# Kernel tuning notes

Measured on AMD Instinct MI355X. Metric: run time of the kernel, lower is better.

## Reference

```python
import jax, jax.numpy as jnp
import numpy as np

N, E, B = 50000, 800000, 64
IN, H, OUT = 64, 128, 64


def _gcn_norm(edge_index, num_nodes):
    # PyG gcn_norm with add_self_loops=True: A_hat = A + I, norm = d^-1/2[src]*d^-1/2[dst]
    loop = jnp.arange(num_nodes)
    src = jnp.concatenate([edge_index[0], loop])
    dst = jnp.concatenate([edge_index[1], loop])
    deg = jax.ops.segment_sum(jnp.ones_like(dst, dtype=jnp.float32), dst,
                              num_segments=num_nodes)  # >= 1 due to self-loops
    dis = deg ** -0.5
    norm = dis[src] * dis[dst]  # [E+N]
    return src, dst, norm


def _gcn_layer(x, W, b, src, dst, norm, num_nodes):
    h = x @ W                                   # linear first (GCNConv order)
    msg = h[src] * norm[:, None]                # gather + normalize, [E+N, H]
    out = jax.ops.segment_sum(msg, dst, num_segments=num_nodes)  # scatter-add
    return out + b


def setup_inputs() -> dict:
    key = jax.random.key(0)
    ks = jax.random.split(key, 12)
    x = jax.random.normal(ks[0], (N, IN), dtype=jnp.float32)
    edge_index = jax.random.randint(ks[1], (2, E), 0, N, dtype=jnp.int64)
    batch = jnp.sort(jax.random.randint(ks[2], (N,), 0, B, dtype=jnp.int64))

    def lin(k, fan_in, fan_out):
        s = 1.0 / np.sqrt(fan_in)
        return jax.random.uniform(k, (fan_in, fan_out), jnp.float32, -s, s)

    return {
        "x": x, "edge_index": edge_index, "batch": batch,
        "W1": lin(ks[3], IN, H), "b1": jnp.zeros((H,), jnp.float32),
        "W2": lin(ks[4], H, H),  "b2": jnp.zeros((H,), jnp.float32),
        "W3": lin(ks[5], H, H),  "b3": jnp.zeros((H,), jnp.float32),
        "W4": lin(ks[6], H, OUT), "b4": jnp.zeros((OUT,), jnp.float32),
    }


def reference(x, edge_index, batch, W1, b1, W2, b2, W3, b3, W4, b4):
    src, dst, norm = _gcn_norm(edge_index, N)
    h = jax.nn.relu(_gcn_layer(x, W1, b1, src, dst, norm, N))
    h = jax.nn.relu(_gcn_layer(h, W2, b2, src, dst, norm, N))
    # global mean pool over graphs
    sums = jax.ops.segment_sum(h, batch, num_segments=B)          # [B, H]
    cnts = jax.ops.segment_sum(jnp.ones((N,), jnp.float32), batch, num_segments=B)
    pooled = sums / jnp.maximum(cnts, 1.0)[:, None]
    # MLP head
    return jax.nn.relu(pooled @ W3 + b3) @ W4 + b4                # [B, OUT]
```

## Files before the change

### kernel.cpp

```cpp
#include <hip/hip_runtime.h>


__device__ __forceinline__ float ldf(const void* p, long long i, int f32) {
    if (f32) return ((const float*)p)[i];
    unsigned int u = ((const unsigned short*)p)[i];
    return __uint_as_float(u << 16);
}
__device__ __forceinline__ float bfl(unsigned int u) { return __uint_as_float(u << 16); }
__device__ __forceinline__ float bfh(unsigned int u) { return __uint_as_float(u & 0xFFFF0000u); }
__device__ __forceinline__ int ld_idx(const int* p, long long i, int i64) {
    return i64 ? p[2 * i] : p[i];
}
__device__ __forceinline__ unsigned short f2bf(float v) {
    unsigned int x = __float_as_uint(v);
    return (unsigned short)((x + 0x7FFFu + ((x >> 16) & 1u)) >> 16);
}
__device__ __forceinline__ int clampi(int v, int lo, int hi) {
    return v < lo ? lo : (v > hi ? hi : v);
}

#define OW1 0
#define OB1 8192
#define OW2 8320
#define OB2 24704
#define OW3 24832
#define OB3 41216
#define OW4 41344
#define OB4 49536
#define OTOT 49600


__global__ void gnn_prep(const void* W1, const void* b1, const void* W2, const void* b2,
                         const void* W3, const void* b3, const void* W4, const void* b4,
                         const int* __restrict__ ei,
                         int* __restrict__ flags_out,
                         int* __restrict__ degcnt, float* __restrict__ pooled,
                         float* __restrict__ wsW, int N, int B) {
    __shared__ int s_cnt, s_or;
    const int t = threadIdx.x;
    if (t == 0) { s_cnt = 0; s_or = 0; }
    __syncthreads();
    {
        const unsigned int* w1w = (const unsigned int*)W1;
        int c = 0, o = 0;
        for (int i = t; i < 512; i += 256) {
            unsigned int e = (w1w[i] >> 7) & 0xFFu;
            if (e >= 100 && e <= 140) c++;
        }
        for (int i = t; i < 1024; i += 256) o |= ei[2 * i + 1];
        atomicAdd(&s_cnt, c);
        atomicOr(&s_or, o);
    }
    __syncthreads();
    const int f32 = (s_cnt > 256) ? 0 : 1;
    if (blockIdx.x == 0 && t == 0) {
        flags_out[0] = f32;
        flags_out[1] = (s_or == 0) ? 1 : 0;
    }
    const int i = blockIdx.x * 256 + t;
    const int stride = gridDim.x * 256;
    for (int j = i; j < N; j += stride) degcnt[j] = 0;
    for (int j = i; j < B * 128; j += stride) pooled[j] = 0.f;
    for (int j = i; j < OTOT; j += stride) {
        float v;
        if      (j < OB1) v = ldf(W1, j - OW1, f32);
        else if (j < OW2) v = ldf(b1, j - OB1, f32);
        else if (j < OB2) v = ldf(W2, j - OW2, f32);
        else if (j < OW3) v = ldf(b2, j - OB2, f32);
        else if (j < OB3) v = ldf(W3, j - OW3, f32);
        else if (j < OW4) v = ldf(b3, j - OB3, f32);
        else if (j < OB4) v = ldf(W4, j - OW4, f32);
        else              v = ldf(b4, j - OB4, f32);
        wsW[j] = v;
    }
}


__global__ void gnn_hist(const int* __restrict__ ei, int E, int N,
                         const int* __restrict__ flags, int* __restrict__ degcnt,
                         int* __restrict__ rank) {
    int base = (blockIdx.x * 256 + threadIdx.x) * 4;
    if (base >= E) return;
    int i64 = flags[1];
    int m = min(4, E - base);
    int d[4], r[4];
#pragma unroll
    for (int j = 0; j < 4; ++j)
        if (j < m) d[j] = clampi(ld_idx(ei, (long long)E + base + j, i64), 0, N - 1);
#pragma unroll
    for (int j = 0; j < 4; ++j)
        if (j < m) r[j] = atomicAdd(&degcnt[d[j]], 1);
#pragma unroll
    for (int j = 0; j < 4; ++j)
        if (j < m) rank[base + j] = r[j];
}

__global__ void gnn_scan1(const int* __restrict__ cnt, int* __restrict__ excl,
                          int* __restrict__ sums, float* __restrict__ dis, int N) {
    __shared__ int sh[256];
    int t = threadIdx.x;
    int i = blockIdx.x * 256 + t;
    int v = (i < N) ? cnt[i] : 0;
    sh[t] = v;
    __syncthreads();
    for (int off = 1; off < 256; off <<= 1) {
        int a = (t >= off) ? sh[t - off] : 0;
        __syncthreads();
        sh[t] += a;
        __syncthreads();
    }
    if (i < N) {
        excl[i] = sh[t] - v;
        dis[i] = rsqrtf((float)v + 1.0f);
    }
    if (t == 255) sums[blockIdx.x] = sh[255];
}

__global__ void gnn_scan2(int* __restrict__ sums, int nb) {
    __shared__ int sh[256];
    int t = threadIdx.x;
    int v = (t < nb) ? sums[t] : 0;
    sh[t] = v;
    __syncthreads();
    for (int off = 1; off < 256; off <<= 1) {
        int a = (t >= off) ? sh[t - off] : 0;
        __syncthreads();
        sh[t] += a;
        __syncthreads();
    }
    if (t < nb) sums[t] = sh[t] - v;
}

template <bool SMALLN>
__global__ void gnn_fill(const int* __restrict__ ei, const int* __restrict__ excl,
                         const int* __restrict__ bsums, const int* __restrict__ rank,
                         void* __restrict__ csr, int E, int N,
                         const int* __restrict__ flags,
                         const void* __restrict__ x, const float* __restrict__ dis,
                         unsigned short* __restrict__ xb) {
    const int tid = blockIdx.x * 256 + threadIdx.x;
    const int i64 = flags[1];
    if (tid < E) {
        int s = clampi(ld_idx(ei, (long long)tid, i64), 0, N - 1);
        int d = clampi(ld_idx(ei, (long long)E + tid, i64), 0, N - 1);
        int pos = excl[d] + bsums[d >> 8] + rank[tid];
        if (SMALLN) ((unsigned short*)csr)[pos] = (unsigned short)s;
        else        ((int*)csr)[pos] = s;
    }
    const int f32 = flags[0];
    const int total = N * 16;
    const int stride = gridDim.x * 256;
    for (int j = tid; j < total; j += stride) {
        int n = j >> 4;
        float dn = dis[n];
        float v0, v1, v2, v3;
        if (f32) {
            float4 xv = ((const float4*)x)[j];
            v0 = xv.x; v1 = xv.y; v2 = xv.z; v3 = xv.w;
        } else {
            ushort4 xv = ((const ushort4*)x)[j];
            v0 = bfl(xv.x); v1 = bfl(xv.y); v2 = bfl(xv.z); v3 = bfl(xv.w);
        }
        ushort4 o;
        o.x = f2bf(v0 * dn); o.y = f2bf(v1 * dn);
        o.z = f2bf(v2 * dn); o.w = f2bf(v3 * dn);
        ((ushort4*)xb)[j] = o;
    }
}

template <bool SMALLN>
__device__ __forceinline__ int csr_at(const void* csr, int e) {
    return SMALLN ? (int)((const unsigned short*)csr)[e] : ((const int*)csr)[e];
}


template <bool SMALLN>
__global__ __launch_bounds__(128) void gnn_l1l2(const unsigned short* __restrict__ xb,
                                                const int* __restrict__ excl,
                                                const int* __restrict__ bsums,
                                                const void* __restrict__ csr,
                                                const float* __restrict__ dis,
                                                const float* __restrict__ W1,
                                                const float* __restrict__ b1,
                                                const float* __restrict__ W2,
                                                int N, int E,
                                                unsigned short* __restrict__ A2) {
    __shared__ float Xs[16 * 68];
    __shared__ float Hs[16 * 128];
    const int t = threadIdx.x;
    const int nbase = blockIdx.x * 16;
    const int lane = t & 63;
    const int nd = (t >> 6) * 8 + (lane >> 3);
    const int fg = lane & 7;
    const int n = nbase + nd;

    if (n < N) {
        const float dn = dis[n];
        uint4 us = *(const uint4*)(xb + (long long)n * 64 + fg * 8);
        float a0 = bfl(us.x), a1 = bfh(us.x), a2 = bfl(us.y), a3 = bfh(us.y);
        float a4 = bfl(us.z), a5 = bfh(us.z), a6 = bfl(us.w), a7 = bfh(us.w);
        int beg = excl[n] + bsums[n >> 8];
        int end = (n + 1 < N) ? (excl[n + 1] + bsums[(n + 1) >> 8]) : E;
        int e = beg;
        for (; e + 4 <= end; e += 4) {
            int s0 = csr_at<SMALLN>(csr, e),     s1 = csr_at<SMALLN>(csr, e + 1);
            int s2 = csr_at<SMALLN>(csr, e + 2), s3 = csr_at<SMALLN>(csr, e + 3);
            uint4 u0 = *(const uint4*)(xb + (long long)s0 * 64 + fg * 8);
            uint4 u1 = *(const uint4*)(xb + (long long)s1 * 64 + fg * 8);
            uint4 u2 = *(const uint4*)(xb + (long long)s2 * 64 + fg * 8);
            uint4 u3 = *(const uint4*)(xb + (long long)s3 * 64 + fg * 8);
            a0 += bfl(u0.x); a1 += bfh(u0.x); a2 += bfl(u0.y); a3 += bfh(u0.y);
            a4 += bfl(u0.z); a5 += bfh(u0.z); a6 += bfl(u0.w); a7 += bfh(u0.w);
            a0 += bfl(u1.x); a1 += bfh(u1.x); a2 += bfl(u1.y); a3 += bfh(u1.y);
            a4 += bfl(u1.z); a5 += bfh(u1.z); a6 += bfl(u1.w); a7 += bfh(u1.w);
            a0 += bfl(u2.x); a1 += bfh(u2.x); a2 += bfl(u2.y); a3 += bfh(u2.y);
            a4 += bfl(u2.z); a5 += bfh(u2.z); a6 += bfl(u2.w); a7 += bfh(u2.w);
            a0 += bfl(u3.x); a1 += bfh(u3.x); a2 += bfl(u3.y); a3 += bfh(u3.y);
            a4 += bfl(u3.z); a5 += bfh(u3.z); a6 += bfl(u3.w); a7 += bfh(u3.w);
        }
        for (; e < end; ++e) {
            int s = csr_at<SMALLN>(csr, e);
            uint4 u = *(const uint4*)(xb + (long long)s * 64 + fg * 8);
            a0 += bfl(u.x); a1 += bfh(u.x); a2 += bfl(u.y); a3 += bfh(u.y);
            a4 += bfl(u.z); a5 += bfh(u.z); a6 += bfl(u.w); a7 += bfh(u.w);
        }
        float4 o0, o1;
        o0.x = a0 * dn; o0.y = a1 * dn; o0.z = a2 * dn; o0.w = a3 * dn;
        o1.x = a4 * dn; o1.y = a5 * dn; o1.z = a6 * dn; o1.w = a7 * dn;
        *(float4*)&Xs[nd * 68 + fg * 8]     = o0;
        *(float4*)&Xs[nd * 68 + fg * 8 + 4] = o1;
    } else {
        float4 z = make_float4(0.f, 0.f, 0.f, 0.f);
        *(float4*)&Xs[nd * 68 + fg * 8]     = z;
        *(float4*)&Xs[nd * 68 + fg * 8 + 4] = z;
    }
    __syncthreads();

    const int fgB = t & 31, ng = t >> 5;
    const int f0 = fgB * 4, n0 = ng * 4;
    {
        const float4* Wp = (const float4*)W1;
        float4 acc[4];
#pragma unroll
        for (int j = 0; j < 4; ++j) acc[j] = make_float4(0.f, 0.f, 0.f, 0.f);
#pragma unroll 4
        for (int k4 = 0; k4 < 16; ++k4) {
            const float4 wa = Wp[(4 * k4 + 0) * 32 + fgB];
            const float4 wb = Wp[(4 * k4 + 1) * 32 + fgB];
            const float4 wc = Wp[(4 * k4 + 2) * 32 + fgB];
            const float4 wd = Wp[(4 * k4 + 3) * 32 + fgB];
#pragma unroll
            for (int j = 0; j < 4; ++j) {
                const float4 xv = *(const float4*)&Xs[(n0 + j) * 68 + k4 * 4];
                acc[j].x = fmaf(xv.x, wa.x, acc[j].x); acc[j].y = fmaf(xv.x, wa.y, acc[j].y);
                acc[j].z = fmaf(xv.x, wa.z, acc[j].z); acc[j].w = fmaf(xv.x, wa.w, acc[j].w);
                acc[j].x = fmaf(xv.y, wb.x, acc[j].x); acc[j].y = fmaf(xv.y, wb.y, acc[j].y);
                acc[j].z = fmaf(xv.y, wb.z, acc[j].z); acc[j].w = fmaf(xv.y, wb.w, acc[j].w);
                acc[j].x = fmaf(xv.z, wc.x, acc[j].x); acc[j].y = fmaf(xv.z, wc.y, acc[j].y);
                acc[j].z = fmaf(xv.z, wc.z, acc[j].z); acc[j].w = fmaf(xv.z, wc.w, acc[j].w);
                acc[j].x = fmaf(xv.w, wd.x, acc[j].x); acc[j].y = fmaf(xv.w, wd.y, acc[j].y);
                acc[j].z = fmaf(xv.w, wd.z, acc[j].z); acc[j].w = fmaf(xv.w, wd.w, acc[j].w);
            }
        }
        const float4 b = *(const float4*)&b1[f0];
#pragma unroll
        for (int j = 0; j < 4; ++j) {
            float4 a = acc[j];
            a.x = fmaxf(a.x + b.x, 0.f);
            a.y = fmaxf(a.y + b.y, 0.f);
            a.z = fmaxf(a.z + b.z, 0.f);
            a.w = fmaxf(a.w + b.w, 0.f);
            *(float4*)&Hs[(n0 + j) * 128 + f0] = a;
        }
    }
    __syncthreads();
    {
        const float4* Wp = (const float4*)W2;
        float4 acc[4];
#pragma unroll
        for (int j = 0; j < 4; ++j) acc[j] = make_float4(0.f, 0.f, 0.f, 0.f);
#pragma unroll 4
        for (int k4 = 0; k4 < 32; ++k4) {
            const float4 wa = Wp[(4 * k4 + 0) * 32 + fgB];
            const float4 wb = Wp[(4 * k4 + 1) * 32 + fgB];
            const float4 wc = Wp[(4 * k4 + 2) * 32 + fgB];
            const float4 wd = Wp[(4 * k4 + 3) * 32 + fgB];
#pragma unroll
            for (int j = 0; j < 4; ++j) {
                const float4 xv = *(const float4*)&Hs[(n0 + j) * 128 + k4 * 4];
                acc[j].x = fmaf(xv.x, wa.x, acc[j].x); acc[j].y = fmaf(xv.x, wa.y, acc[j].y);
                acc[j].z = fmaf(xv.x, wa.z, acc[j].z); acc[j].w = fmaf(xv.x, wa.w, acc[j].w);
                acc[j].x = fmaf(xv.y, wb.x, acc[j].x); acc[j].y = fmaf(xv.y, wb.y, acc[j].y);
                acc[j].z = fmaf(xv.y, wb.z, acc[j].z); acc[j].w = fmaf(xv.y, wb.w, acc[j].w);
                acc[j].x = fmaf(xv.z, wc.x, acc[j].x); acc[j].y = fmaf(xv.z, wc.y, acc[j].y);
                acc[j].z = fmaf(xv.z, wc.z, acc[j].z); acc[j].w = fmaf(xv.z, wc.w, acc[j].w);
                acc[j].x = fmaf(xv.w, wd.x, acc[j].x); acc[j].y = fmaf(xv.w, wd.y, acc[j].y);
                acc[j].z = fmaf(xv.w, wd.z, acc[j].z); acc[j].w = fmaf(xv.w, wd.w, acc[j].w);
            }
        }
#pragma unroll
        for (int j = 0; j < 4; ++j) {
            int nn = nbase + n0 + j;
            if (nn >= N) continue;
            const float dn = dis[nn];
            float4 a = acc[j];
            a.x *= dn; a.y *= dn; a.z *= dn; a.w *= dn;
            uint2 u;
            u.x = (unsigned int)f2bf(a.x) | ((unsigned int)f2bf(a.y) << 16);
            u.y = (unsigned int)f2bf(a.z) | ((unsigned int)f2bf(a.w) << 16);
            *(uint2*)(A2 + (long long)nn * 128 + f0) = u;
        }
    }
}


template <bool SMALLN>
__global__ __launch_bounds__(256) void gnn_agg_bf(const unsigned short* __restrict__ A2,
                                                  const int* __restrict__ excl,
                                                  const int* __restrict__ bsums,
                                                  const void* __restrict__ csr,
                                                  const float* __restrict__ dis,
                                                  const float* __restrict__ bias,
                                                  float* __restrict__ outC, int N, int E) {
    const int t = threadIdx.x;
    const int lane = t & 63;
    const int n = blockIdx.x * 16 + (t >> 6) * 4 + (lane >> 4);
    if (n >= N) return;
    const int fg = lane & 15;
    const float dn = dis[n];
    uint4 us = *(const uint4*)(A2 + (long long)n * 128 + fg * 8);
    float a0 = bfl(us.x), a1 = bfh(us.x), a2 = bfl(us.y), a3 = bfh(us.y);
    float a4 = bfl(us.z), a5 = bfh(us.z), a6 = bfl(us.w), a7 = bfh(us.w);
    int beg = excl[n] + bsums[n >> 8];
    int end = (n + 1 < N) ? (excl[n + 1] + bsums[(n + 1) >> 8]) : E;
    int e = beg;
    for (; e + 4 <= end; e += 4) {
        int s0 = csr_at<SMALLN>(csr, e),     s1 = csr_at<SMALLN>(csr, e + 1);
        int s2 = csr_at<SMALLN>(csr, e + 2), s3 = csr_at<SMALLN>(csr, e + 3);
        uint4 u0 = *(const uint4*)(A2 + (long long)s0 * 128 + fg * 8);
        uint4 u1 = *(const uint4*)(A2 + (long long)s1 * 128 + fg * 8);
        uint4 u2 = *(const uint4*)(A2 + (long long)s2 * 128 + fg * 8);
        uint4 u3 = *(const uint4*)(A2 + (long long)s3 * 128 + fg * 8);
        a0 += bfl(u0.x); a1 += bfh(u0.x); a2 += bfl(u0.y); a3 += bfh(u0.y);
        a4 += bfl(u0.z); a5 += bfh(u0.z); a6 += bfl(u0.w); a7 += bfh(u0.w);
        a0 += bfl(u1.x); a1 += bfh(u1.x); a2 += bfl(u1.y); a3 += bfh(u1.y);
        a4 += bfl(u1.z); a5 += bfh(u1.z); a6 += bfl(u1.w); a7 += bfh(u1.w);
        a0 += bfl(u2.x); a1 += bfh(u2.x); a2 += bfl(u2.y); a3 += bfh(u2.y);
        a4 += bfl(u2.z); a5 += bfh(u2.z); a6 += bfl(u2.w); a7 += bfh(u2.w);
        a0 += bfl(u3.x); a1 += bfh(u3.x); a2 += bfl(u3.y); a3 += bfh(u3.y);
        a4 += bfl(u3.z); a5 += bfh(u3.z); a6 += bfl(u3.w); a7 += bfh(u3.w);
    }
    for (; e < end; ++e) {
        int s = csr_at<SMALLN>(csr, e);
        uint4 u = *(const uint4*)(A2 + (long long)s * 128 + fg * 8);
        a0 += bfl(u.x); a1 += bfh(u.x); a2 += bfl(u.y); a3 += bfh(u.y);
        a4 += bfl(u.z); a5 += bfh(u.z); a6 += bfl(u.w); a7 += bfh(u.w);
    }
    const float4 bA = *(const float4*)&bias[fg * 8];
    const float4 bB = *(const float4*)&bias[fg * 8 + 4];
    float4 o0, o1;
    o0.x = fmaxf(a0 * dn + bA.x, 0.f);
    o0.y = fmaxf(a1 * dn + bA.y, 0.f);
    o0.z = fmaxf(a2 * dn + bA.z, 0.f);
    o0.w = fmaxf(a3 * dn + bA.w, 0.f);
    o1.x = fmaxf(a4 * dn + bB.x, 0.f);
    o1.y = fmaxf(a5 * dn + bB.y, 0.f);
    o1.z = fmaxf(a6 * dn + bB.z, 0.f);
    o1.w = fmaxf(a7 * dn + bB.w, 0.f);
    *(float4*)(outC + (long long)n * 128 + fg * 8)     = o0;
    *(float4*)(outC + (long long)n * 128 + fg * 8 + 4) = o1;
}


#define PSTRIP 32
__global__ __launch_bounds__(128) void gnn_pool(const float* __restrict__ h,
                                                const int* __restrict__ batch,
                                                const int* __restrict__ flags,
                                                float* __restrict__ pooled, int N, int B) {
    int i64 = flags[1];
    int f = threadIdx.x;
    int n0 = blockIdx.x * PSTRIP;
    if (n0 >= N) return;
    int nend = min(n0 + PSTRIP, N);
    int cur = clampi(ld_idx(batch, n0, i64), 0, B - 1);
    float acc = 0.0f;
    for (int n = n0; n < nend; ++n) {
        int b = clampi(ld_idx(batch, n, i64), 0, B - 1);
        if (b != cur) {
            atomicAdd(&pooled[cur * 128 + f], acc);
            acc = 0.0f; cur = b;
        }
        acc += h[(long long)n * 128 + f];
    }
    atomicAdd(&pooled[cur * 128 + f], acc);
}


__global__ __launch_bounds__(128) void gnn_head(const float* __restrict__ pooled,
                                                const int* __restrict__ batch,
                                                const float* __restrict__ W3,
                                                const float* __restrict__ b3,
                                                const float* __restrict__ W4,
                                                const float* __restrict__ b4,
                                                const int* __restrict__ flags,
                                                void* __restrict__ outv, int N) {
    __shared__ float xs[128];
    __shared__ float rs[128];
    __shared__ float cinv;
    int b = blockIdx.x, f = threadIdx.x;
    if (f == 0) {
        int i64 = flags[1];
        int L = 0, R = N;
        while (L < R) { int m = (L + R) >> 1; if (ld_idx(batch, m, i64) < b) L = m + 1; else R = m; }
        int lo = L;
        L = 0; R = N;
        while (L < R) { int m = (L + R) >> 1; if (ld_idx(batch, m, i64) < b + 1) L = m + 1; else R = m; }
        cinv = 1.0f / fmaxf((float)(L - lo), 1.0f);
    }
    __syncthreads();
    xs[f] = pooled[b * 128 + f] * cinv;
    __syncthreads();
    float acc = b3[f];
    for (int k = 0; k < 128; ++k) acc = fmaf(xs[k], W3[k * 128 + f], acc);
    rs[f] = fmaxf(acc, 0.f);
    __syncthreads();
    if (f < 64) {
        float a2 = b4[f];
        for (int k = 0; k < 128; ++k) a2 = fmaf(rs[k], W4[k * 64 + f], a2);
        if (flags[0]) ((float*)outv)[b * 64 + f] = a2;
        else          ((unsigned short*)outv)[b * 64 + f] = f2bf(a2);
    }
}


extern "C" void kernel_launch(void* const* d_in, const int* in_sizes, int n_in,
                              void* d_out, int out_size, void* d_ws, size_t ws_size,
                              hipStream_t stream) {
    const void* x  = d_in[0];
    const int* ei  = (const int*)d_in[1];
    const int* bat = (const int*)d_in[2];

    const int N = in_sizes[0] / 64;
    const int E = in_sizes[1] / 2;
    const int B = out_size / 64;
    const bool smalln = (N < 65536);

    char* p = (char*)d_ws;
    auto alloc = [&](size_t bytes) { void* q = (void*)p; p += (bytes + 255) & ~(size_t)255; return q; };
    int*   flags    = (int*)alloc(256);
    float* wsW      = (float*)alloc((size_t)OTOT * 4);
    int*   degcnt   = (int*)alloc((size_t)N * 4);
    float* dis      = (float*)alloc((size_t)N * 4);
    int*   excl     = (int*)alloc((size_t)N * 4);
    int*   bsums    = (int*)alloc(1024);
    int*   rank     = (int*)alloc((size_t)E * 4);
    void*  csr      = alloc((size_t)E * (smalln ? 2 : 4));
    unsigned short* xb = (unsigned short*)alloc((size_t)N * 64 * 2);
    float* C2       = (float*)alloc((size_t)N * 128 * 4);
    unsigned short* A2 = (unsigned short*)alloc((size_t)N * 128 * 2);
    float* pooled   = (float*)alloc((size_t)B * 128 * 4);
    (void)ws_size; (void)n_in;

    const int nbN = (N + 255) / 256;

    gnn_prep<<<512, 256, 0, stream>>>(d_in[3], d_in[4], d_in[5], d_in[6],
                                      d_in[7], d_in[8], d_in[9], d_in[10],
                                      ei, flags, degcnt, pooled, wsW, N, B);

    gnn_hist<<<(E + 1023) / 1024, 256, 0, stream>>>(ei, E, N, flags, degcnt, rank);
    gnn_scan1<<<nbN, 256, 0, stream>>>(degcnt, excl, bsums, dis, N);
    gnn_scan2<<<1, 256, 0, stream>>>(bsums, nbN);
    if (smalln)
        gnn_fill<true><<<(E + 255) / 256, 256, 0, stream>>>(ei, excl, bsums, rank, csr, E, N,
                                                            flags, x, dis, xb);
    else
        gnn_fill<false><<<(E + 255) / 256, 256, 0, stream>>>(ei, excl, bsums, rank, csr, E, N,
                                                             flags, x, dis, xb);

    const int nblk = (N + 15) / 16;

    if (smalln)
        gnn_l1l2<true><<<nblk, 128, 0, stream>>>(xb, excl, bsums, csr, dis,
                                                 wsW + OW1, wsW + OB1, wsW + OW2, N, E, A2);
    else
        gnn_l1l2<false><<<nblk, 128, 0, stream>>>(xb, excl, bsums, csr, dis,
                                                  wsW + OW1, wsW + OB1, wsW + OW2, N, E, A2);

    if (smalln)
        gnn_agg_bf<true><<<nblk, 256, 0, stream>>>(A2, excl, bsums, csr, dis, wsW + OB2, C2, N, E);
    else
        gnn_agg_bf<false><<<nblk, 256, 0, stream>>>(A2, excl, bsums, csr, dis, wsW + OB2, C2, N, E);

    gnn_pool<<<(N + PSTRIP - 1) / PSTRIP, 128, 0, stream>>>(C2, bat, flags, pooled, N, B);
    gnn_head<<<B, 128, 0, stream>>>(pooled, bat, wsW + OW3, wsW + OB3,
                                    wsW + OW4, wsW + OB4, flags, d_out, N);
}
```

Measured before the change: 261.7 us.

## Split each node's edge list across thread slots and reduce with shuffles

Both gather-aggregation kernels now split each node's neighbour list across several thread groups (2 slots in the fused layer-1/2 kernel, 4 slots in the layer-2 aggregation) and combine the partial sums with cross-lane shuffles. The fused kernel doubles its block to 256 threads, and its dense transform stage halves the rows handled per thread to match. The goal is more memory-level parallelism for the random row gathers, since each node averages about 17 edges. The cost is extra shuffle work, idle lanes on low-degree nodes, and higher thread counts per node.

```diff
diff --git a/kernel.cpp b/kernel.cpp
--- a/kernel.cpp
+++ b/kernel.cpp
@@ -175,7 +175,7 @@
 
 
 template <bool SMALLN>
-__global__ __launch_bounds__(128) void gnn_l1l2(const unsigned short* __restrict__ xb,
+__global__ __launch_bounds__(256) void gnn_l1l2(const unsigned short* __restrict__ xb,
                                                 const int* __restrict__ excl,
                                                 const int* __restrict__ bsums,
                                                 const void* __restrict__ csr,
@@ -189,22 +189,25 @@
     __shared__ float Hs[16 * 128];
     const int t = threadIdx.x;
     const int nbase = blockIdx.x * 16;
-    const int lane = t & 63;
-    const int nd = (t >> 6) * 8 + (lane >> 3);
-    const int fg = lane & 7;
+    const int nd = t >> 4;
+    const int eslot = (t >> 3) & 1;
+    const int fg = t & 7;
     const int n = nbase + nd;
 
+    float a0 = 0.f, a1 = 0.f, a2 = 0.f, a3 = 0.f;
+    float a4 = 0.f, a5 = 0.f, a6 = 0.f, a7 = 0.f;
     if (n < N) {
-        const float dn = dis[n];
-        uint4 us = *(const uint4*)(xb + (long long)n * 64 + fg * 8);
-        float a0 = bfl(us.x), a1 = bfh(us.x), a2 = bfl(us.y), a3 = bfh(us.y);
-        float a4 = bfl(us.z), a5 = bfh(us.z), a6 = bfl(us.w), a7 = bfh(us.w);
+        if (eslot == 1) {
+            uint4 us = *(const uint4*)(xb + (long long)n * 64 + fg * 8);
+            a0 = bfl(us.x); a1 = bfh(us.x); a2 = bfl(us.y); a3 = bfh(us.y);
+            a4 = bfl(us.z); a5 = bfh(us.z); a6 = bfl(us.w); a7 = bfh(us.w);
+        }
         int beg = excl[n] + bsums[n >> 8];
         int end = (n + 1 < N) ? (excl[n + 1] + bsums[(n + 1) >> 8]) : E;
-        int e = beg;
-        for (; e + 4 <= end; e += 4) {
-            int s0 = csr_at<SMALLN>(csr, e),     s1 = csr_at<SMALLN>(csr, e + 1);
-            int s2 = csr_at<SMALLN>(csr, e + 2), s3 = csr_at<SMALLN>(csr, e + 3);
+        int e = beg + eslot;
+        for (; e + 6 < end; e += 8) {
+            int s0 = csr_at<SMALLN>(csr, e),     s1 = csr_at<SMALLN>(csr, e + 2);
+            int s2 = csr_at<SMALLN>(csr, e + 4), s3 = csr_at<SMALLN>(csr, e + 6);
             uint4 u0 = *(const uint4*)(xb + (long long)s0 * 64 + fg * 8);
             uint4 u1 = *(const uint4*)(xb + (long long)s1 * 64 + fg * 8);
             uint4 u2 = *(const uint4*)(xb + (long long)s2 * 64 + fg * 8);
@@ -218,31 +221,34 @@
             a0 += bfl(u3.x); a1 += bfh(u3.x); a2 += bfl(u3.y); a3 += bfh(u3.y);
             a4 += bfl(u3.z); a5 += bfh(u3.z); a6 += bfl(u3.w); a7 += bfh(u3.w);
         }
-        for (; e < end; ++e) {
+        for (; e < end; e += 2) {
             int s = csr_at<SMALLN>(csr, e);
             uint4 u = *(const uint4*)(xb + (long long)s * 64 + fg * 8);
             a0 += bfl(u.x); a1 += bfh(u.x); a2 += bfl(u.y); a3 += bfh(u.y);
             a4 += bfl(u.z); a5 += bfh(u.z); a6 += bfl(u.w); a7 += bfh(u.w);
         }
+    }
+    a0 += __shfl_xor(a0, 8); a1 += __shfl_xor(a1, 8);
+    a2 += __shfl_xor(a2, 8); a3 += __shfl_xor(a3, 8);
+    a4 += __shfl_xor(a4, 8); a5 += __shfl_xor(a5, 8);
+    a6 += __shfl_xor(a6, 8); a7 += __shfl_xor(a7, 8);
+    if (eslot == 0) {
+        const float dn = (n < N) ? dis[n] : 0.f;
         float4 o0, o1;
         o0.x = a0 * dn; o0.y = a1 * dn; o0.z = a2 * dn; o0.w = a3 * dn;
         o1.x = a4 * dn; o1.y = a5 * dn; o1.z = a6 * dn; o1.w = a7 * dn;
         *(float4*)&Xs[nd * 68 + fg * 8]     = o0;
         *(float4*)&Xs[nd * 68 + fg * 8 + 4] = o1;
-    } else {
-        float4 z = make_float4(0.f, 0.f, 0.f, 0.f);
-        *(float4*)&Xs[nd * 68 + fg * 8]     = z;
-        *(float4*)&Xs[nd * 68 + fg * 8 + 4] = z;
     }
     __syncthreads();
 
     const int fgB = t & 31, ng = t >> 5;
-    const int f0 = fgB * 4, n0 = ng * 4;
+    const int f0 = fgB * 4, n0 = ng * 2;
     {
         const float4* Wp = (const float4*)W1;
-        float4 acc[4];
-#pragma unroll
-        for (int j = 0; j < 4; ++j) acc[j] = make_float4(0.f, 0.f, 0.f, 0.f);
+        float4 acc[2];
+#pragma unroll
+        for (int j = 0; j < 2; ++j) acc[j] = make_float4(0.f, 0.f, 0.f, 0.f);
 #pragma unroll 4
         for (int k4 = 0; k4 < 16; ++k4) {
             const float4 wa = Wp[(4 * k4 + 0) * 32 + fgB];
@@ -250,7 +256,7 @@
             const float4 wc = Wp[(4 * k4 + 2) * 32 + fgB];
             const float4 wd = Wp[(4 * k4 + 3) * 32 + fgB];
 #pragma unroll
-            for (int j = 0; j < 4; ++j) {
+            for (int j = 0; j < 2; ++j) {
                 const float4 xv = *(const float4*)&Xs[(n0 + j) * 68 + k4 * 4];
                 acc[j].x = fmaf(xv.x, wa.x, acc[j].x); acc[j].y = fmaf(xv.x, wa.y, acc[j].y);
                 acc[j].z = fmaf(xv.x, wa.z, acc[j].z); acc[j].w = fmaf(xv.x, wa.w, acc[j].w);
@@ -264,7 +270,7 @@
         }
         const float4 b = *(const float4*)&b1[f0];
 #pragma unroll
-        for (int j = 0; j < 4; ++j) {
+        for (int j = 0; j < 2; ++j) {
             float4 a = acc[j];
             a.x = fmaxf(a.x + b.x, 0.f);
             a.y = fmaxf(a.y + b.y, 0.f);
@@ -276,9 +282,9 @@
     __syncthreads();
     {
         const float4* Wp = (const float4*)W2;
-        float4 acc[4];
-#pragma unroll
-        for (int j = 0; j < 4; ++j) acc[j] = make_float4(0.f, 0.f, 0.f, 0.f);
+        float4 acc[2];
+#pragma unroll
+        for (int j = 0; j < 2; ++j) acc[j] = make_float4(0.f, 0.f, 0.f, 0.f);
 #pragma unroll 4
         for (int k4 = 0; k4 < 32; ++k4) {
             const float4 wa = Wp[(4 * k4 + 0) * 32 + fgB];
@@ -286,7 +292,7 @@
             const float4 wc = Wp[(4 * k4 + 2) * 32 + fgB];
             const float4 wd = Wp[(4 * k4 + 3) * 32 + fgB];
 #pragma unroll
-            for (int j = 0; j < 4; ++j) {
+            for (int j = 0; j < 2; ++j) {
                 const float4 xv = *(const float4*)&Hs[(n0 + j) * 128 + k4 * 4];
                 acc[j].x = fmaf(xv.x, wa.x, acc[j].x); acc[j].y = fmaf(xv.x, wa.y, acc[j].y);
                 acc[j].z = fmaf(xv.x, wa.z, acc[j].z); acc[j].w = fmaf(xv.x, wa.w, acc[j].w);
@@ -299,7 +305,7 @@
             }
         }
 #pragma unroll
-        for (int j = 0; j < 4; ++j) {
+        for (int j = 0; j < 2; ++j) {
             int nn = nbase + n0 + j;
             if (nn >= N) continue;
             const float dn = dis[nn];
@@ -324,51 +330,66 @@
                                                   float* __restrict__ outC, int N, int E) {
     const int t = threadIdx.x;
     const int lane = t & 63;
-    const int n = blockIdx.x * 16 + (t >> 6) * 4 + (lane >> 4);
-    if (n >= N) return;
+    const int n = blockIdx.x * 4 + (t >> 6);
+    const int eslot = lane >> 4;
     const int fg = lane & 15;
-    const float dn = dis[n];
-    uint4 us = *(const uint4*)(A2 + (long long)n * 128 + fg * 8);
-    float a0 = bfl(us.x), a1 = bfh(us.x), a2 = bfl(us.y), a3 = bfh(us.y);
-    float a4 = bfl(us.z), a5 = bfh(us.z), a6 = bfl(us.w), a7 = bfh(us.w);
-    int beg = excl[n] + bsums[n >> 8];
-    int end = (n + 1 < N) ? (excl[n + 1] + bsums[(n + 1) >> 8]) : E;
-    int e = beg;
-    for (; e + 4 <= end; e += 4) {
-        int s0 = csr_at<SMALLN>(csr, e),     s1 = csr_at<SMALLN>(csr, e + 1);
-        int s2 = csr_at<SMALLN>(csr, e + 2), s3 = csr_at<SMALLN>(csr, e + 3);
-        uint4 u0 = *(const uint4*)(A2 + (long long)s0 * 128 + fg * 8);
-        uint4 u1 = *(const uint4*)(A2 + (long long)s1 * 128 + fg * 8);
-        uint4 u2 = *(const uint4*)(A2 + (long long)s2 * 128 + fg * 8);
-        uint4 u3 = *(const uint4*)(A2 + (long long)s3 * 128 + fg * 8);
-        a0 += bfl(u0.x); a1 += bfh(u0.x); a2 += bfl(u0.y); a3 += bfh(u0.y);
-        a4 += bfl(u0.z); a5 += bfh(u0.z); a6 += bfl(u0.w); a7 += bfh(u0.w);
-        a0 += bfl(u1.x); a1 += bfh(u1.x); a2 += bfl(u1.y); a3 += bfh(u1.y);
-        a4 += bfl(u1.z); a5 += bfh(u1.z); a6 += bfl(u1.w); a7 += bfh(u1.w);
-        a0 += bfl(u2.x); a1 += bfh(u2.x); a2 += bfl(u2.y); a3 += bfh(u2.y);
-        a4 += bfl(u2.z); a5 += bfh(u2.z); a6 += bfl(u2.w); a7 += bfh(u2.w);
-        a0 += bfl(u3.x); a1 += bfh(u3.x); a2 += bfl(u3.y); a3 += bfh(u3.y);
-        a4 += bfl(u3.z); a5 += bfh(u3.z); a6 += bfl(u3.w); a7 += bfh(u3.w);
-    }
-    for (; e < end; ++e) {
-        int s = csr_at<SMALLN>(csr, e);
-        uint4 u = *(const uint4*)(A2 + (long long)s * 128 + fg * 8);
-        a0 += bfl(u.x); a1 += bfh(u.x); a2 += bfl(u.y); a3 += bfh(u.y);
-        a4 += bfl(u.z); a5 += bfh(u.z); a6 += bfl(u.w); a7 += bfh(u.w);
-    }
-    const float4 bA = *(const float4*)&bias[fg * 8];
-    const float4 bB = *(const float4*)&bias[fg * 8 + 4];
-    float4 o0, o1;
-    o0.x = fmaxf(a0 * dn + bA.x, 0.f);
-    o0.y = fmaxf(a1 * dn + bA.y, 0.f);
-    o0.z = fmaxf(a2 * dn + bA.z, 0.f);
-    o0.w = fmaxf(a3 * dn + bA.w, 0.f);
-    o1.x = fmaxf(a4 * dn + bB.x, 0.f);
-    o1.y = fmaxf(a5 * dn + bB.y, 0.f);
-    o1.z = fmaxf(a6 * dn + bB.z, 0.f);
-    o1.w = fmaxf(a7 * dn + bB.w, 0.f);
-    *(float4*)(outC + (long long)n * 128 + fg * 8)     = o0;
-    *(float4*)(outC + (long long)n * 128 + fg * 8 + 4) = o1;
+    float a0 = 0.f, a1 = 0.f, a2 = 0.f, a3 = 0.f;
+    float a4 = 0.f, a5 = 0.f, a6 = 0.f, a7 = 0.f;
+    if (n < N) {
+        if (eslot == 3) {
+            uint4 us = *(const uint4*)(A2 + (long long)n * 128 + fg * 8);
+            a0 = bfl(us.x); a1 = bfh(us.x); a2 = bfl(us.y); a3 = bfh(us.y);
+            a4 = bfl(us.z); a5 = bfh(us.z); a6 = bfl(us.w); a7 = bfh(us.w);
+        }
+        int beg = excl[n] + bsums[n >> 8];
+        int end = (n + 1 < N) ? (excl[n + 1] + bsums[(n + 1) >> 8]) : E;
+        int e = beg + eslot;
+        for (; e + 12 < end; e += 16) {
+            int s0 = csr_at<SMALLN>(csr, e),     s1 = csr_at<SMALLN>(csr, e + 4);
+            int s2 = csr_at<SMALLN>(csr, e + 8), s3 = csr_at<SMALLN>(csr, e + 12);
+            uint4 u0 = *(const uint4*)(A2 + (long long)s0 * 128 + fg * 8);
+            uint4 u1 = *(const uint4*)(A2 + (long long)s1 * 128 + fg * 8);
+            uint4 u2 = *(const uint4*)(A2 + (long long)s2 * 128 + fg * 8);
+            uint4 u3 = *(const uint4*)(A2 + (long long)s3 * 128 + fg * 8);
+            a0 += bfl(u0.x); a1 += bfh(u0.x); a2 += bfl(u0.y); a3 += bfh(u0.y);
+            a4 += bfl(u0.z); a5 += bfh(u0.z); a6 += bfl(u0.w); a7 += bfh(u0.w);
+            a0 += bfl(u1.x); a1 += bfh(u1.x); a2 += bfl(u1.y); a3 += bfh(u1.y);
+            a4 += bfl(u1.z); a5 += bfh(u1.z); a6 += bfl(u1.w); a7 += bfh(u1.w);
+            a0 += bfl(u2.x); a1 += bfh(u2.x); a2 += bfl(u2.y); a3 += bfh(u2.y);
+            a4 += bfl(u2.z); a5 += bfh(u2.z); a6 += bfl(u2.w); a7 += bfh(u2.w);
+            a0 += bfl(u3.x); a1 += bfh(u3.x); a2 += bfl(u3.y); a3 += bfh(u3.y);
+            a4 += bfl(u3.z); a5 += bfh(u3.z); a6 += bfl(u3.w); a7 += bfh(u3.w);
+        }
+        for (; e < end; e += 4) {
+            int s = csr_at<SMALLN>(csr, e);
+            uint4 u = *(const uint4*)(A2 + (long long)s * 128 + fg * 8);
+            a0 += bfl(u.x); a1 += bfh(u.x); a2 += bfl(u.y); a3 += bfh(u.y);
+            a4 += bfl(u.z); a5 += bfh(u.z); a6 += bfl(u.w); a7 += bfh(u.w);
+        }
+    }
+#pragma unroll
+    for (int m = 16; m <= 32; m <<= 1) {
+        a0 += __shfl_xor(a0, m); a1 += __shfl_xor(a1, m);
+        a2 += __shfl_xor(a2, m); a3 += __shfl_xor(a3, m);
+        a4 += __shfl_xor(a4, m); a5 += __shfl_xor(a5, m);
+        a6 += __shfl_xor(a6, m); a7 += __shfl_xor(a7, m);
+    }
+    if (n < N && eslot == 0) {
+        const float dn = dis[n];
+        const float4 bA = *(const float4*)&bias[fg * 8];
+        const float4 bB = *(const float4*)&bias[fg * 8 + 4];
+        float4 o0, o1;
+        o0.x = fmaxf(a0 * dn + bA.x, 0.f);
+        o0.y = fmaxf(a1 * dn + bA.y, 0.f);
+        o0.z = fmaxf(a2 * dn + bA.z, 0.f);
+        o0.w = fmaxf(a3 * dn + bA.w, 0.f);
+        o1.x = fmaxf(a4 * dn + bB.x, 0.f);
+        o1.y = fmaxf(a5 * dn + bB.y, 0.f);
+        o1.z = fmaxf(a6 * dn + bB.z, 0.f);
+        o1.w = fmaxf(a7 * dn + bB.w, 0.f);
+        *(float4*)(outC + (long long)n * 128 + fg * 8)     = o0;
+        *(float4*)(outC + (long long)n * 128 + fg * 8 + 4) = o1;
+    }
 }
 
 
@@ -480,16 +501,18 @@
     const int nblk = (N + 15) / 16;
 
     if (smalln)
-        gnn_l1l2<true><<<nblk, 128, 0, stream>>>(xb, excl, bsums, csr, dis,
+        gnn_l1l2<true><<<nblk, 256, 0, stream>>>(xb, excl, bsums, csr, dis,
                                                  wsW + OW1, wsW + OB1, wsW + OW2, N, E, A2);
     else
-        gnn_l1l2<false><<<nblk, 128, 0, stream>>>(xb, excl, bsums, csr, dis,
+        gnn_l1l2<false><<<nblk, 256, 0, stream>>>(xb, excl, bsums, csr, dis,
                                                   wsW + OW1, wsW + OB1, wsW + OW2, N, E, A2);
 
     if (smalln)
-        gnn_agg_bf<true><<<nblk, 256, 0, stream>>>(A2, excl, bsums, csr, dis, wsW + OB2, C2, N, E);
+        gnn_agg_bf<true><<<(N + 3) / 4, 256, 0, stream>>>(A2, excl, bsums, csr, dis,
+                                                          wsW + OB2, C2, N, E);
     else
-        gnn_agg_bf<false><<<nblk, 256, 0, stream>>>(A2, excl, bsums, csr, dis, wsW + OB2, C2, N, E);
+        gnn_agg_bf<false><<<(N + 3) / 4, 256, 0, stream>>>(A2, excl, bsums, csr, dis,
+                                                           wsW + OB2, C2, N, E);
 
     gnn_pool<<<(N + PSTRIP - 1) / PSTRIP, 128, 0, stream>>>(C2, bat, flags, pooled, N, B);
     gnn_head<<<B, 128, 0, stream>>>(pooled, bat, wsW + OW3, wsW + OB3,
```

New measurement: 284.9 us. 1.09x slower.
